# Optimization experiments

Measured on AMD Instinct MI355X. Metric: run time of the kernel, lower is better.

The kernel has to match this reference:

```python
import jax, jax.numpy as jnp
import numpy as np
from jax import lax

B, T, H, W, C = 2, 16, 64, 64, 64
KT, K = 3, 3


def kernel_to_freq_3d(kernel, T, H, W):
    # kernel: (C, k_t, k_h, k_w) -> (C, T, H, W) complex freq response
    Cc, k_t, k_h, k_w = kernel.shape
    t_idx = (jnp.arange(k_t) - k_t // 2) % T
    h_idx = (jnp.arange(k_h) - k_h // 2) % H
    w_idx = (jnp.arange(k_w) - k_w // 2) % W
    tt, th, tw = jnp.meshgrid(t_idx, h_idx, w_idx, indexing='ij')
    padded = jnp.zeros((Cc, T, H, W), dtype=kernel.dtype).at[:, tt, th, tw].set(kernel)
    return jnp.fft.fftn(padded, axes=(1, 2, 3))


def mamba_op(left, right):
    a1, b1 = left
    a2, b2 = right
    return (a1 * a2, a2 * b1 + b2)


def setup_inputs() -> dict:
    key = jax.random.key(0)
    ks = jax.random.split(key, 8)
    fan_in = KT * K * K
    x = jax.random.normal(ks[0], (B, T, H, W, C), dtype=jnp.float32)
    A_kernel = jax.random.normal(ks[1], (C, KT, K, K), dtype=jnp.float32) / np.sqrt(fan_in)
    B_kernel = jax.random.normal(ks[2], (C, KT, K, K), dtype=jnp.float32) / np.sqrt(fan_in)
    forget_bias = jnp.full((C,), 2.0, dtype=jnp.float32)
    forget_scale = jnp.full((C,), 0.01, dtype=jnp.float32)
    input_bias = jnp.zeros((C,), dtype=jnp.float32)
    input_scale = jnp.full((C,), 0.01, dtype=jnp.float32)
    delta_W = jax.random.normal(ks[3], (C, C), dtype=jnp.float32) / np.sqrt(C)
    delta_b = jnp.zeros((C,), dtype=jnp.float32)
    return {"x": x, "A_kernel": A_kernel, "B_kernel": B_kernel,
            "forget_bias": forget_bias, "forget_scale": forget_scale,
            "input_bias": input_bias, "input_scale": input_scale,
            "delta_W": delta_W, "delta_b": delta_b}


def reference(x, A_kernel, B_kernel, forget_bias, forget_scale,
              input_bias, input_scale, delta_W, delta_b):
    Bb, Tt, Hh, Ww, Cc = x.shape
    # freq-domain kernels: (C,T,H,W) -> (T,1,H,W,C) for broadcasting over batch
    A_f = kernel_to_freq_3d(A_kernel, Tt, Hh, Ww).transpose(1, 2, 3, 0)[:, None]
    B_f = kernel_to_freq_3d(B_kernel, Tt, Hh, Ww).transpose(1, 2, 3, 0)[:, None]
    # input-dependent gates (real, elementwise per channel)
    forget_gate = jax.nn.sigmoid(forget_bias + forget_scale * x)
    input_gate = jax.nn.sigmoid(input_bias + input_scale * x)
    delta = jax.nn.softplus(jnp.einsum('bthwc,cd->bthwd', x, delta_W) + delta_b)
    x_f = jnp.fft.fftn(x, axes=(1, 2, 3))  # complex (B,T,H,W,C)
    # move time axis to front for the scan: (T,B,H,W,C)
    a_seq = forget_gate.transpose(1, 0, 2, 3, 4) * A_f
    b_seq = (input_gate.transpose(1, 0, 2, 3, 4)
             * delta.transpose(1, 0, 2, 3, 4)
             * B_f * x_f.transpose(1, 0, 2, 3, 4))
    _, h_all_f = lax.associative_scan(mamba_op, (a_seq, b_seq), axis=0)
    h_f = h_all_f.transpose(1, 0, 2, 3, 4)
    h = jnp.fft.ifftn(h_f, axes=(1, 2, 3)).real
    return h.astype(x.dtype)
```

## Files before the change

### kernel.cpp

```cpp
#include <hip/hip_runtime.h>
#include <math.h>

#define Bb 2
#define Tt 16
#define Hh 64
#define Ww 64
#define Cc 64
#define ST_ (Hh*Ww*Cc)
#define SH_ (Ww*Cc)
#define SB_ (Tt*Hh*Ww*Cc)

#define TWO_PI 6.2831853071795864769f

typedef __attribute__((ext_vector_type(8))) short bf16x8;
typedef __attribute__((ext_vector_type(4))) float f32x4;

__device__ __forceinline__ float2 cmul(float2 a, float2 b) {
    return make_float2(fmaf(a.x, b.x, -a.y * b.y), fmaf(a.x, b.y, a.y * b.x));
}
__device__ __forceinline__ float2 cadd(float2 a, float2 b) { return make_float2(a.x + b.x, a.y + b.y); }
__device__ __forceinline__ float2 csub(float2 a, float2 b) { return make_float2(a.x - b.x, a.y - b.y); }

__device__ __forceinline__ unsigned bfpack(float2 f) {
    unsigned r = __float_as_uint(f.x);
    unsigned i = __float_as_uint(f.y);
    r = (r + 0x7fffu + ((r >> 16) & 1u)) >> 16;
    i = (i + 0x7fffu + ((i >> 16) & 1u)) >> 16;
    return r | (i << 16);
}
__device__ __forceinline__ float2 bfunpack(unsigned u) {
    return make_float2(__uint_as_float(u << 16), __uint_as_float(u & 0xffff0000u));
}

template <int S>
__device__ __forceinline__ void fft8(float2 v[8]) {
    const float R = 0.70710678118654752f;
    float2 s0 = cadd(v[0], v[4]), d0 = csub(v[0], v[4]);
    float2 s1 = cadd(v[1], v[5]), d1 = csub(v[1], v[5]);
    float2 s2 = cadd(v[2], v[6]), d2 = csub(v[2], v[6]);
    float2 s3 = cadd(v[3], v[7]), d3 = csub(v[3], v[7]);
    d1 = make_float2(R * (d1.x - (float)S * d1.y), R * ((float)S * d1.x + d1.y));
    { float2 t = d2; d2 = make_float2(-(float)S * t.y, (float)S * t.x); }
    d3 = make_float2(R * (-d3.x - (float)S * d3.y), R * ((float)S * d3.x - d3.y));
    float2 u0 = cadd(s0, s2), u2 = csub(s0, s2);
    float2 u1 = cadd(s1, s3), u3t = csub(s1, s3);
    float2 u3 = make_float2(-(float)S * u3t.y, (float)S * u3t.x);
    v[0] = cadd(u0, u1); v[1] = csub(u0, u1); v[2] = cadd(u2, u3); v[3] = csub(u2, u3);
    float2 w0 = cadd(d0, d2), w2 = csub(d0, d2);
    float2 w1 = cadd(d1, d3), w3t = csub(d1, d3);
    float2 w3 = make_float2(-(float)S * w3t.y, (float)S * w3t.x);
    v[4] = cadd(w0, w1); v[5] = csub(w0, w1); v[6] = cadd(w2, w3); v[7] = csub(w2, w3);
}

template <int S>
__device__ __forceinline__ void fft4(float2& a, float2& b, float2& c, float2& d) {
    float2 t0 = cadd(a, c), t1 = csub(a, c);
    float2 t2 = cadd(b, d), t3 = csub(b, d);
    a = cadd(t0, t2);
    c = csub(t0, t2);
    b = make_float2(t1.x - (float)S * t3.y, t1.y + (float)S * t3.x);
    d = make_float2(t1.x + (float)S * t3.y, t1.y - (float)S * t3.x);
}

template <int S>
__device__ __forceinline__ void fft16(float2 v[16]) {
    const float CS[10] = {1.f, 0.92387953f, 0.70710678f, 0.38268343f, 0.f,
                          -0.38268343f, -0.70710678f, -0.92387953f, -1.f, -0.92387953f};
    const float SN[10] = {0.f, 0.38268343f, 0.70710678f, 0.92387953f, 1.f,
                          0.92387953f, 0.70710678f, 0.38268343f, 0.f, -0.38268343f};
    float2 A[4][4];
#pragma unroll
    for (int j = 0; j < 4; ++j) {
        A[j][0] = v[j]; A[j][1] = v[4 + j]; A[j][2] = v[8 + j]; A[j][3] = v[12 + j];
        fft4<S>(A[j][0], A[j][1], A[j][2], A[j][3]);
#pragma unroll
        for (int k0 = 0; k0 < 4; ++k0) {
            int m = j * k0;
            float2 tw = make_float2(CS[m], (float)S * SN[m]);
            A[j][k0] = cmul(A[j][k0], tw);
        }
    }
#pragma unroll
    for (int k0 = 0; k0 < 4; ++k0) {
        fft4<S>(A[0][k0], A[1][k0], A[2][k0], A[3][k0]);
        v[k0] = A[0][k0]; v[k0 + 4] = A[1][k0]; v[k0 + 8] = A[2][k0]; v[k0 + 12] = A[3][k0];
    }
}

__global__ __launch_bounds__(256) void k_fft_w_fwd(const float* __restrict__ x,
                                                   unsigned* __restrict__ X) {
    __shared__ float2 ex[64 * 65];
    const int brev[8] = {0, 4, 2, 6, 1, 5, 3, 7};
    int tid = threadIdx.x;
    int j = tid >> 5, cl = tid & 31;
    int base = blockIdx.x * 4096;
    float2 v[2][8];
#pragma unroll
    for (int q = 0; q < 2; ++q) {
        int c = cl + 32 * q;
#pragma unroll
        for (int n1 = 0; n1 < 8; ++n1)
            v[q][n1] = make_float2(x[base + (8 * n1 + j) * 64 + c], 0.f);
    }
    float sj, cj; sincosf(-TWO_PI * (float)j / 64.f, &sj, &cj);
    float2 w1 = make_float2(cj, sj);
#pragma unroll
    for (int q = 0; q < 2; ++q) {
        fft8<-1>(v[q]);
        int c = cl + 32 * q;
        float2 tw = make_float2(1.f, 0.f);
#pragma unroll
        for (int k0 = 0; k0 < 8; ++k0) {
            ex[c * 65 + j * 8 + k0] = cmul(v[q][brev[k0]], tw);
            tw = cmul(tw, w1);
        }
    }
    __syncthreads();
#pragma unroll
    for (int q = 0; q < 2; ++q) {
        int c = cl + 32 * q;
        float2 z[8];
#pragma unroll
        for (int n0 = 0; n0 < 8; ++n0) z[n0] = ex[c * 65 + n0 * 8 + j];
        fft8<-1>(z);
#pragma unroll
        for (int m = 0; m < 8; ++m)
            X[base + (j + 8 * brev[m]) * 64 + c] = bfpack(z[m]);
    }
}

template <int S, int SHIFT>
__global__ __launch_bounds__(256) void k_fft_h(unsigned* __restrict__ X) {
    __shared__ float2 ex[64 * 65];
    const int brev[8] = {0, 4, 2, 6, 1, 5, 3, 7};
    const float sc = 1.0f / (float)(1 << SHIFT);
    int tid = threadIdx.x;
    int j = tid >> 5, cl = tid & 31;
    int s = blockIdx.x;
    int bt = s >> 6, w = s & 63;
    int base = bt * ST_ + w * 64;
    float2 v[2][8];
#pragma unroll
    for (int q = 0; q < 2; ++q) {
        int c = cl + 32 * q;
#pragma unroll
        for (int n1 = 0; n1 < 8; ++n1)
            v[q][n1] = bfunpack(X[base + (8 * n1 + j) * SH_ + c]);
    }
    float sj, cj; sincosf((float)S * TWO_PI * (float)j / 64.f, &sj, &cj);
    float2 w1 = make_float2(cj, sj);
#pragma unroll
    for (int q = 0; q < 2; ++q) {
        fft8<S>(v[q]);
        int c = cl + 32 * q;
        float2 tw = make_float2(1.f, 0.f);
#pragma unroll
        for (int k0 = 0; k0 < 8; ++k0) {
            ex[c * 65 + j * 8 + k0] = cmul(v[q][brev[k0]], tw);
            tw = cmul(tw, w1);
        }
    }
    __syncthreads();
#pragma unroll
    for (int q = 0; q < 2; ++q) {
        int c = cl + 32 * q;
        float2 z[8];
#pragma unroll
        for (int n0 = 0; n0 < 8; ++n0) z[n0] = ex[c * 65 + n0 * 8 + j];
        fft8<S>(z);
#pragma unroll
        for (int m = 0; m < 8; ++m) {
            float2 o = make_float2(z[m].x * sc, z[m].y * sc);
            X[base + (j + 8 * brev[m]) * SH_ + c] = bfpack(o);
        }
    }
}

__global__ __launch_bounds__(256) void k_mid(
    const float* __restrict__ x, unsigned* __restrict__ X,
    const float* __restrict__ Ak, const float* __restrict__ Bk,
    const float* __restrict__ fb, const float* __restrict__ fs,
    const float* __restrict__ ib, const float* __restrict__ isc_,
    const float* __restrict__ dW, const float* __restrict__ db) {
    const float CT[16] = {1.f, 0.9238795f, 0.7071068f, 0.3826834f, 0.f, -0.3826834f,
                          -0.7071068f, -0.9238795f, -1.f, -0.9238795f, -0.7071068f,
                          -0.3826834f, 0.f, 0.3826834f, 0.7071068f, 0.9238795f};
    const float SN[16] = {0.f, 0.3826834f, 0.7071068f, 0.9238795f, 1.f, 0.9238795f,
                          0.7071068f, 0.3826834f, 0.f, -0.3826834f, -0.7071068f,
                          -0.9238795f, -1.f, -0.9238795f, -0.7071068f, -0.3826834f};
    __shared__ float Wl[4096];
    __shared__ float Akl[1728], Bkl[1728];
    __shared__ __align__(16) float xs[4][16 * 68 + 4];

    int tid = threadIdx.x;
    int g = tid >> 6, lane = tid & 63;
    int c = lane;
    int site = blockIdx.x * 4 + g;
    int b = site >> 12, hw = site & 4095;
    int h = hw >> 6, w = hw & 63;
    int base = b * SB_ + hw * 64;

    for (int i = tid; i < 4096; i += 256) Wl[i] = dW[i];
    for (int i = tid; i < 1728; i += 256) { Akl[i] = Ak[i]; Bkl[i] = Bk[i]; }

    float xv[16];
    float2 v[16];
#pragma unroll
    for (int t = 0; t < 16; ++t) {
        xv[t] = x[base + t * ST_ + c];
        v[t] = bfunpack(X[base + t * ST_ + c]);
    }
#pragma unroll
    for (int t = 0; t < 16; ++t) xs[g][t * 68 + c] = xv[t];
    __syncthreads();

    int m = lane & 15, q = lane >> 4;
    bf16x8 Afrag[2];
#pragma unroll
    for (int ka = 0; ka < 2; ++ka) {
        int d0 = ka * 32 + q * 8;
        const float* p = &xs[g][m * 68 + d0];
        float4 f0 = *(const float4*)p;
        float4 f1 = *(const float4*)(p + 4);
        union { bf16x8 v8; unsigned u[4]; } U;
        U.u[0] = bfpack(make_float2(f0.x, f0.y));
        U.u[1] = bfpack(make_float2(f0.z, f0.w));
        U.u[2] = bfpack(make_float2(f1.x, f1.y));
        U.u[3] = bfpack(make_float2(f1.z, f1.w));
        Afrag[ka] = U.v8;
    }
#pragma unroll
    for (int nt = 0; nt < 4; ++nt) {
        int ccol = m + 16 * nt;
        float dbn = db[ccol];
        f32x4 acc = {dbn, dbn, dbn, dbn};
#pragma unroll
        for (int ka = 0; ka < 2; ++ka) {
            int kb = ka * 32 + q * 8;
            union { bf16x8 v8; unsigned u[4]; } Ub;
#pragma unroll
            for (int p2 = 0; p2 < 4; ++p2)
                Ub.u[p2] = bfpack(make_float2(Wl[(kb + 2 * p2) * 64 + ccol],
                                              Wl[(kb + 2 * p2 + 1) * 64 + ccol]));
            acc = __builtin_amdgcn_mfma_f32_16x16x32_bf16(Afrag[ka], Ub.v8, acc, 0, 0, 0);
        }
#pragma unroll
        for (int reg = 0; reg < 4; ++reg)
            xs[g][(q * 4 + reg) * 68 + ccol] = acc[reg];
    }

    float sh, ch; sincosf(TWO_PI * (float)h / 64.0f, &sh, &ch);
    float sw, cw; sincosf(TWO_PI * (float)w / 64.0f, &sw, &cw);
    float2 eh[3] = { make_float2(ch, sh), make_float2(1.f, 0.f), make_float2(ch, -sh) };
    float2 ew[3] = { make_float2(cw, sw), make_float2(1.f, 0.f), make_float2(cw, -sw) };
    float2 GA[3], GB[3];
#pragma unroll
    for (int kt = 0; kt < 3; ++kt) { GA[kt] = make_float2(0.f, 0.f); GB[kt] = make_float2(0.f, 0.f); }
#pragma unroll
    for (int kh = 0; kh < 3; ++kh) {
#pragma unroll
        for (int kw = 0; kw < 3; ++kw) {
            float2 e = cmul(eh[kh], ew[kw]);
#pragma unroll
            for (int kt = 0; kt < 3; ++kt) {
                float ka = Akl[c * 27 + kt * 9 + kh * 3 + kw];
                float kb = Bkl[c * 27 + kt * 9 + kh * 3 + kw];
                GA[kt].x = fmaf(ka, e.x, GA[kt].x);
                GA[kt].y = fmaf(ka, e.y, GA[kt].y);
                GB[kt].x = fmaf(kb, e.x, GB[kt].x);
                GB[kt].y = fmaf(kb, e.y, GB[kt].y);
            }
        }
    }
    float fbc = fb[c], fsc = fs[c], ibc = ib[c], iscv = isc_[c];

    fft16<-1>(v);
    __syncthreads();

    float delta_raw[16];
#pragma unroll
    for (int t = 0; t < 16; ++t) delta_raw[t] = xs[g][t * 68 + c];

    float2 hv = make_float2(0.f, 0.f);
#pragma unroll
    for (int t = 0; t < 16; ++t) {
        float ct = CT[t], st = SN[t];
        float2 Af, Bf;
        Af.x = GA[1].x + ct * (GA[0].x + GA[2].x) - st * (GA[0].y - GA[2].y);
        Af.y = GA[1].y + ct * (GA[0].y + GA[2].y) + st * (GA[0].x - GA[2].x);
        Bf.x = GB[1].x + ct * (GB[0].x + GB[2].x) - st * (GB[0].y - GB[2].y);
        Bf.y = GB[1].y + ct * (GB[0].y + GB[2].y) + st * (GB[0].x - GB[2].x);

        float xc = xv[t];
        float fg  = __builtin_amdgcn_rcpf(1.f + __expf(-(fbc + fsc * xc)));
        float igv = __builtin_amdgcn_rcpf(1.f + __expf(-(ibc + iscv * xc)));
        float dot = delta_raw[t];
        float delta = (dot > 20.f) ? dot : __logf(1.f + __expf(dot));

        float sR = igv * delta;
        float2 bbv;
        bbv.x = sR * (Bf.x * v[t].x - Bf.y * v[t].y);
        bbv.y = sR * (Bf.x * v[t].y + Bf.y * v[t].x);
        float2 av = make_float2(fg * Af.x, fg * Af.y);
        float2 nh;
        nh.x = av.x * hv.x - av.y * hv.y + bbv.x;
        nh.y = av.x * hv.y + av.y * hv.x + bbv.y;
        hv = nh;
        v[t] = hv;
    }

    fft16<1>(v);

#pragma unroll
    for (int t = 0; t < 16; ++t) {
        float2 o = make_float2(v[t].x * 0.0625f, v[t].y * 0.0625f);
        X[base + t * ST_ + c] = bfpack(o);
    }
}

__global__ __launch_bounds__(256) void k_fft_w_inv_out(const unsigned* __restrict__ X,
                                                       float* __restrict__ out) {
    __shared__ float2 ex[64 * 65];
    const int brev[8] = {0, 4, 2, 6, 1, 5, 3, 7};
    int tid = threadIdx.x;
    int j = tid >> 5, cl = tid & 31;
    int base = blockIdx.x * 4096;
    float2 v[2][8];
#pragma unroll
    for (int q = 0; q < 2; ++q) {
        int c = cl + 32 * q;
#pragma unroll
        for (int n1 = 0; n1 < 8; ++n1)
            v[q][n1] = bfunpack(X[base + (8 * n1 + j) * 64 + c]);
    }
    float sj, cj; sincosf(TWO_PI * (float)j / 64.f, &sj, &cj);
    float2 w1 = make_float2(cj, sj);
#pragma unroll
    for (int q = 0; q < 2; ++q) {
        fft8<1>(v[q]);
        int c = cl + 32 * q;
        float2 tw = make_float2(1.f, 0.f);
#pragma unroll
        for (int k0 = 0; k0 < 8; ++k0) {
            ex[c * 65 + j * 8 + k0] = cmul(v[q][brev[k0]], tw);
            tw = cmul(tw, w1);
        }
    }
    __syncthreads();
#pragma unroll
    for (int q = 0; q < 2; ++q) {
        int c = cl + 32 * q;
        float2 z[8];
#pragma unroll
        for (int n0 = 0; n0 < 8; ++n0) z[n0] = ex[c * 65 + n0 * 8 + j];
        fft8<1>(z);
#pragma unroll
        for (int m = 0; m < 8; ++m)
            out[base + (j + 8 * brev[m]) * 64 + c] = z[m].x * (1.0f / 64.0f);
    }
}

extern "C" void kernel_launch(void* const* d_in, const int* in_sizes, int n_in,
                              void* d_out, int out_size, void* d_ws, size_t ws_size,
                              hipStream_t stream) {
    const float* x   = (const float*)d_in[0];
    const float* Ak  = (const float*)d_in[1];
    const float* Bk  = (const float*)d_in[2];
    const float* fb  = (const float*)d_in[3];
    const float* fs  = (const float*)d_in[4];
    const float* ib  = (const float*)d_in[5];
    const float* is_ = (const float*)d_in[6];
    const float* dW  = (const float*)d_in[7];
    const float* db  = (const float*)d_in[8];
    float* out = (float*)d_out;
    unsigned* X = (unsigned*)d_ws;

    k_fft_w_fwd<<<Bb * Tt * Hh, 256, 0, stream>>>(x, X);
    k_fft_h<-1, 0><<<Bb * Tt * Ww, 256, 0, stream>>>(X);
    k_mid<<<(Bb * Hh * Ww) / 4, 256, 0, stream>>>(x, X, Ak, Bk, fb, fs, ib, is_, dW, db);
    k_fft_h<1, 6><<<Bb * Tt * Ww, 256, 0, stream>>>(X);
    k_fft_w_inv_out<<<Bb * Tt * Hh, 256, 0, stream>>>(X, out);
}
```

Measured before the change: 174.2 us.

## Store FFT exchange buffers as packed bf16 and prepack delta_W fragments

Shared-memory exchange buffers in the four FFT kernels now hold packed bf16 complex values (4 bytes) instead of float2, halving LDS use so more blocks can be resident, and launch bounds request 4 blocks per CU. The first block of the forward W-FFT also packs delta_W into MFMA B-fragment layout in workspace. k_mid then loads those fragments directly instead of staging the 16KB weight matrix in LDS and converting it per block. The extra bf16 rounding between FFT stages lowers accuracy, and the workspace must be large enough to hold the prepacked weights.

New measurement: 173.6 us. No clear change (-0.4%).

```diff
diff --git a/kernel.cpp b/kernel.cpp
--- a/kernel.cpp
+++ b/kernel.cpp
@@ -9,6 +9,7 @@
 #define ST_ (Hh*Ww*Cc)
 #define SH_ (Ww*Cc)
 #define SB_ (Tt*Hh*Ww*Cc)
+#define XELEMS (Bb*Tt*Hh*Ww*Cc)
 
 #define TWO_PI 6.2831853071795864769f
 
@@ -87,11 +88,23 @@
     }
 }
 
-__global__ __launch_bounds__(256) void k_fft_w_fwd(const float* __restrict__ x,
-                                                   unsigned* __restrict__ X) {
-    __shared__ float2 ex[64 * 65];
+__global__ __launch_bounds__(256, 4) void k_fft_w_fwd(const float* __restrict__ x,
+                                                      unsigned* __restrict__ X,
+                                                      const float* __restrict__ dW,
+                                                      unsigned* __restrict__ pre) {
+    __shared__ unsigned ex[64 * 65];
     const int brev[8] = {0, 4, 2, 6, 1, 5, 3, 7};
     int tid = threadIdx.x;
+
+    if (blockIdx.x == 0) {
+        for (int i = tid; i < 2048; i += 256) {
+            int p2 = i & 3, lane = (i >> 2) & 63, ka = (i >> 8) & 1, nt = i >> 9;
+            int kb = ka * 32 + (lane >> 4) * 8 + 2 * p2;
+            int ccol = (lane & 15) + 16 * nt;
+            pre[i] = bfpack(make_float2(dW[kb * 64 + ccol], dW[(kb + 1) * 64 + ccol]));
+        }
+    }
+
     int j = tid >> 5, cl = tid & 31;
     int base = blockIdx.x * 4096;
     float2 v[2][8];
@@ -111,7 +124,7 @@
         float2 tw = make_float2(1.f, 0.f);
 #pragma unroll
         for (int k0 = 0; k0 < 8; ++k0) {
-            ex[c * 65 + j * 8 + k0] = cmul(v[q][brev[k0]], tw);
+            ex[c * 65 + j * 8 + k0] = bfpack(cmul(v[q][brev[k0]], tw));
             tw = cmul(tw, w1);
         }
     }
@@ -121,7 +134,7 @@
         int c = cl + 32 * q;
         float2 z[8];
 #pragma unroll
-        for (int n0 = 0; n0 < 8; ++n0) z[n0] = ex[c * 65 + n0 * 8 + j];
+        for (int n0 = 0; n0 < 8; ++n0) z[n0] = bfunpack(ex[c * 65 + n0 * 8 + j]);
         fft8<-1>(z);
 #pragma unroll
         for (int m = 0; m < 8; ++m)
@@ -130,8 +143,8 @@
 }
 
 template <int S, int SHIFT>
-__global__ __launch_bounds__(256) void k_fft_h(unsigned* __restrict__ X) {
-    __shared__ float2 ex[64 * 65];
+__global__ __launch_bounds__(256, 4) void k_fft_h(unsigned* __restrict__ X) {
+    __shared__ unsigned ex[64 * 65];
     const int brev[8] = {0, 4, 2, 6, 1, 5, 3, 7};
     const float sc = 1.0f / (float)(1 << SHIFT);
     int tid = threadIdx.x;
@@ -156,7 +169,7 @@
         float2 tw = make_float2(1.f, 0.f);
 #pragma unroll
         for (int k0 = 0; k0 < 8; ++k0) {
-            ex[c * 65 + j * 8 + k0] = cmul(v[q][brev[k0]], tw);
+            ex[c * 65 + j * 8 + k0] = bfpack(cmul(v[q][brev[k0]], tw));
             tw = cmul(tw, w1);
         }
     }
@@ -166,7 +179,7 @@
         int c = cl + 32 * q;
         float2 z[8];
 #pragma unroll
-        for (int n0 = 0; n0 < 8; ++n0) z[n0] = ex[c * 65 + n0 * 8 + j];
+        for (int n0 = 0; n0 < 8; ++n0) z[n0] = bfunpack(ex[c * 65 + n0 * 8 + j]);
         fft8<S>(z);
 #pragma unroll
         for (int m = 0; m < 8; ++m) {
@@ -181,14 +194,13 @@
     const float* __restrict__ Ak, const float* __restrict__ Bk,
     const float* __restrict__ fb, const float* __restrict__ fs,
     const float* __restrict__ ib, const float* __restrict__ isc_,
-    const float* __restrict__ dW, const float* __restrict__ db) {
+    const uint4* __restrict__ pre, const float* __restrict__ db) {
     const float CT[16] = {1.f, 0.9238795f, 0.7071068f, 0.3826834f, 0.f, -0.3826834f,
                           -0.7071068f, -0.9238795f, -1.f, -0.9238795f, -0.7071068f,
                           -0.3826834f, 0.f, 0.3826834f, 0.7071068f, 0.9238795f};
     const float SN[16] = {0.f, 0.3826834f, 0.7071068f, 0.9238795f, 1.f, 0.9238795f,
                           0.7071068f, 0.3826834f, 0.f, -0.3826834f, -0.7071068f,
                           -0.9238795f, -1.f, -0.9238795f, -0.7071068f, -0.3826834f};
-    __shared__ float Wl[4096];
     __shared__ float Akl[1728], Bkl[1728];
     __shared__ __align__(16) float xs[4][16 * 68 + 4];
 
@@ -200,7 +212,6 @@
     int h = hw >> 6, w = hw & 63;
     int base = b * SB_ + hw * 64;
 
-    for (int i = tid; i < 4096; i += 256) Wl[i] = dW[i];
     for (int i = tid; i < 1728; i += 256) { Akl[i] = Ak[i]; Bkl[i] = Bk[i]; }
 
     float xv[16];
@@ -236,12 +247,8 @@
         f32x4 acc = {dbn, dbn, dbn, dbn};
 #pragma unroll
         for (int ka = 0; ka < 2; ++ka) {
-            int kb = ka * 32 + q * 8;
-            union { bf16x8 v8; unsigned u[4]; } Ub;
-#pragma unroll
-            for (int p2 = 0; p2 < 4; ++p2)
-                Ub.u[p2] = bfpack(make_float2(Wl[(kb + 2 * p2) * 64 + ccol],
-                                              Wl[(kb + 2 * p2 + 1) * 64 + ccol]));
+            union { bf16x8 v8; uint4 u4; } Ub;
+            Ub.u4 = pre[(nt * 2 + ka) * 64 + lane];
             acc = __builtin_amdgcn_mfma_f32_16x16x32_bf16(Afrag[ka], Ub.v8, acc, 0, 0, 0);
         }
 #pragma unroll
@@ -318,9 +325,9 @@
     }
 }
 
-__global__ __launch_bounds__(256) void k_fft_w_inv_out(const unsigned* __restrict__ X,
-                                                       float* __restrict__ out) {
-    __shared__ float2 ex[64 * 65];
+__global__ __launch_bounds__(256, 4) void k_fft_w_inv_out(const unsigned* __restrict__ X,
+                                                          float* __restrict__ out) {
+    __shared__ unsigned ex[64 * 65];
     const int brev[8] = {0, 4, 2, 6, 1, 5, 3, 7};
     int tid = threadIdx.x;
     int j = tid >> 5, cl = tid & 31;
@@ -342,7 +349,7 @@
         float2 tw = make_float2(1.f, 0.f);
 #pragma unroll
         for (int k0 = 0; k0 < 8; ++k0) {
-            ex[c * 65 + j * 8 + k0] = cmul(v[q][brev[k0]], tw);
+            ex[c * 65 + j * 8 + k0] = bfpack(cmul(v[q][brev[k0]], tw));
             tw = cmul(tw, w1);
         }
     }
@@ -352,7 +359,7 @@
         int c = cl + 32 * q;
         float2 z[8];
 #pragma unroll
-        for (int n0 = 0; n0 < 8; ++n0) z[n0] = ex[c * 65 + n0 * 8 + j];
+        for (int n0 = 0; n0 < 8; ++n0) z[n0] = bfunpack(ex[c * 65 + n0 * 8 + j]);
         fft8<1>(z);
 #pragma unroll
         for (int m = 0; m < 8; ++m)
@@ -374,10 +381,12 @@
     const float* db  = (const float*)d_in[8];
     float* out = (float*)d_out;
     unsigned* X = (unsigned*)d_ws;
-
-    k_fft_w_fwd<<<Bb * Tt * Hh, 256, 0, stream>>>(x, X);
+    unsigned* pre = (unsigned*)((char*)d_ws + (size_t)XELEMS * 4);
+
+    k_fft_w_fwd<<<Bb * Tt * Hh, 256, 0, stream>>>(x, X, dW, pre);
     k_fft_h<-1, 0><<<Bb * Tt * Ww, 256, 0, stream>>>(X);
-    k_mid<<<(Bb * Hh * Ww) / 4, 256, 0, stream>>>(x, X, Ak, Bk, fb, fs, ib, is_, dW, db);
+    k_mid<<<(Bb * Hh * Ww) / 4, 256, 0, stream>>>(x, X, Ak, Bk, fb, fs, ib, is_,
+                                                  (const uint4*)pre, db);
     k_fft_h<1, 6><<<Bb * Tt * Ww, 256, 0, stream>>>(X);
     k_fft_w_inv_out<<<Bb * Tt * Hh, 256, 0, stream>>>(X, out);
 }
```
